# Kernel optimization log

Measured on AMD Instinct MI355X. Metric: run time of the kernel, lower is better.

Reference implementation:

```python
import jax, jax.numpy as jnp
import numpy as np


def _conv_same(x, k):
    # x: [C, H, W] single sample; k: [C_out, C_in, 3, 3] per-sample kernel
    return jax.lax.conv_general_dilated(
        x[None], k, window_strides=(1, 1), padding='SAME',
        dimension_numbers=('NCHW', 'OIHW', 'NCHW'))[0]


_batched_conv = jax.vmap(_conv_same)  # maps over batch of inputs and batch of kernels


def setup_inputs() -> dict:
    key = jax.random.key(0)
    k1, k2, k3 = jax.random.split(key, 3)
    B, C, H, W = 16, 256, 64, 64
    x = jax.random.normal(k1, (B, C, H, W), dtype=jnp.float32)
    # scale kernels down so pre-relu activations stay in a sane range
    kernel1 = jax.random.normal(k2, (B, C, C, 3, 3), dtype=jnp.float32) * 0.02
    kernel2 = jax.random.normal(k3, (B, C, C, 3, 3), dtype=jnp.float32) * 0.02
    return {"x": x, "kernel1": kernel1, "kernel2": kernel2}


def reference(x, kernel1, kernel2):
    # per-sample conv1 -> relu -> per-sample conv2 -> residual add -> relu
    h = jax.nn.relu(_batched_conv(x, kernel1))          # [B, C, H, W]
    out = jax.nn.relu(x + _batched_conv(h, kernel2))    # [B, C, H, W]
    return out
```

## Files before the change

### kernel.cpp

```cpp
#include <hip/hip_runtime.h>
#include <hip/hip_bf16.h>
#include <stdint.h>

typedef __attribute__((ext_vector_type(8))) short bf16x8;
typedef __attribute__((ext_vector_type(4))) float f32x4;
typedef __attribute__((address_space(1))) const void g_void;
typedef __attribute__((address_space(3))) void l_void;

#define NB 16
#define NC 256
#define NHW 4096
#define NT 72
#define ASLOT 8192
#define KSLOT 8192
#define SLOTB (ASLOT + KSLOT)

__global__ __launch_bounds__(256) void prep_xt2(const float* __restrict__ x,
                                                __hip_bfloat16* __restrict__ xt2) {
  __shared__ float tile[64][65];
  const int b = blockIdx.z;
  const int cb = blockIdx.y << 6;
  const int pb = blockIdx.x << 6;
  const float* xs = x + ((size_t)(b * NC + cb) << 12) + pb;
#pragma unroll
  for (int k = 0; k < 16; ++k) {
    int idx = threadIdx.x + (k << 8);
    int c = idx >> 6, p = idx & 63;
    tile[p][c] = xs[((size_t)c << 12) + p];
  }
  __syncthreads();
#pragma unroll
  for (int k = 0; k < 16; ++k) {
    int idx = threadIdx.x + (k << 8);
    int p = idx >> 6, c = idx & 63;
    int P = pb + p, C = cb + c;
    xt2[((size_t)(b * 8 + (C >> 5)) << 17) + ((size_t)P << 5) + (C & 31)] =
        __float2bfloat16(tile[p][c]);
  }
}

__global__ __launch_bounds__(256) void prep_kt2(const float* __restrict__ kin,
                                                __hip_bfloat16* __restrict__ kt2) {
  const int bco = blockIdx.x;
  const int b = bco >> 8, co = bco & 255;
  const size_t base = (size_t)bco * 2304;
  const int ci = threadIdx.x;
  float v[9];
#pragma unroll
  for (int s = 0; s < 9; ++s) v[s] = kin[base + ci * 9 + s];
  const int cib = ci >> 5, chunk = (ci >> 3) & 3, e = ci & 7;
  const int row = co & 127, ct = co >> 7;
  const int sc = chunk ^ ((row >> 1) & 3);
#pragma unroll
  for (int s = 0; s < 9; ++s) {
    const size_t dst = (((size_t)(b * 2 + ct) * NT + (cib * 9 + s)) << 12) +
                       (row << 5) + (sc << 3) + e;
    kt2[dst] = __float2bfloat16(v[s]);
  }
}

__global__ void zero_zp(float* zp) { zp[blockIdx.x * 256 + threadIdx.x] = 0.f; }

template <int PASS>
__global__ __launch_bounds__(256, 3) void conv_gemm(
    const __hip_bfloat16* __restrict__ img2,
    const __hip_bfloat16* __restrict__ kt2,
    const float* __restrict__ xres,
    const __hip_bfloat16* __restrict__ zp,
    void* __restrict__ outp) {
  __shared__ __align__(16) char L[3 * SLOTB];

  const int tid = threadIdx.x;
  const int lane = tid & 63;
  const int wid = tid >> 6;
  const int wm = wid >> 1, wn = wid & 1;

  const int orig = blockIdx.x;
  const int g = ((orig & 7) << 7) + (orig >> 3);
  const int b = g >> 6;
  const int t = g & 63;
  const int ptile = t >> 1;
  const int ct = t & 1;
  const int pbase = ptile << 7;

  const char* xb = (const char*)img2 + ((size_t)b << 21);
  const char* ktb = (const char*)kt2 + (((size_t)(b * 2 + ct) * NT) << 13);
  const char* zpb = (const char*)zp;

  const int srow = lane >> 2;
  const int sch = (lane & 3) ^ ((srow >> 1) & 3);

  const int wI = (PASS == 1) ? wm : wn;
  const int wK = (PASS == 1) ? wn : wm;
  int ioff[4], koff[4];
#pragma unroll
  for (int f = 0; f < 4; ++f) {
    const int ir = (wI << 6) + (f << 4) + (lane & 15);
    ioff[f] = (ir << 6) + ((((lane >> 4) ^ ((ir >> 1) & 3))) << 4);
    const int kr = (wK << 6) + (f << 4) + (lane & 15);
    koff[f] = (kr << 6) + ((((lane >> 4) ^ ((kr >> 1) & 3))) << 4);
  }
  const bool killlo = (lane & 15) == 0;
  const bool killhi = (lane & 15) == 15;
  const bf16x8 z8 = {0, 0, 0, 0, 0, 0, 0, 0};

  f32x4 acc[4][4];
#pragma unroll
  for (int i = 0; i < 4; ++i)
#pragma unroll
    for (int j = 0; j < 4; ++j) acc[i][j] = (f32x4){0.f, 0.f, 0.f, 0.f};

  auto stageA = [&](int slot, int cibp, int dh, int dw, bool dummy) {
    const char* cb = xb + ((size_t)(cibp & 7) << 18);
#pragma unroll
    for (int i = 0; i < 2; ++i) {
      const int grp = (i << 2) + wid;
      const int h = (ptile << 1) + (grp >> 2) + dh;
      const bool ok = !dummy && ((unsigned)h < 64u);
      const int off = ((pbase + (grp << 4) + srow + (dh << 6) + dw) << 6) + (sch << 4);
      const char* src = ok ? cb + off : zpb + (lane << 4);
      __builtin_amdgcn_global_load_lds((g_void*)src,
                                       (l_void*)(L + slot * SLOTB + (grp << 10)), 16, 0, 0);
    }
  };
  auto stageK = [&](int slot, int tn) {
    const char* src0 = ktb + ((size_t)tn << 13);
#pragma unroll
    for (int i = 0; i < 2; ++i) {
      const int grp = (i << 2) + wid;
      const char* src = (tn < NT) ? src0 + (grp << 10) + (lane << 4) : zpb + (lane << 4);
      __builtin_amdgcn_global_load_lds(
          (g_void*)src, (l_void*)(L + slot * SLOTB + ASLOT + (grp << 10)), 16, 0, 0);
    }
  };

  stageA(0, 0, -1, -1, false);
  stageK(0, 0);
  stageA(1, 0, -1, 0, false);
  stageK(1, 1);

#pragma unroll 1
  for (int cib = 0; cib < 8; ++cib) {
#pragma unroll
    for (int s = 0; s < 9; ++s) {
      const int kk = cib * 9 + s;
      asm volatile("s_waitcnt vmcnt(4)" ::: "memory");
      __builtin_amdgcn_s_barrier();
      {
        const int s2 = (s + 2) % 9;
        const int cib2 = cib + (s + 2) / 9;
        const int tn = kk + 2;
        stageA(tn % 3, cib2, s2 / 3 - 1, s2 % 3 - 1, tn >= NT);
        stageK(tn % 3, tn);
      }

      const char* As = L + (kk % 3) * SLOTB;
      const char* Ks = As + ASLOT;
      bf16x8 fi[4], fk[4];
#pragma unroll
      for (int f = 0; f < 4; ++f) fi[f] = *(const bf16x8*)(As + ioff[f]);
#pragma unroll
      for (int f = 0; f < 4; ++f) fk[f] = *(const bf16x8*)(Ks + koff[f]);
      const int dw = s % 3 - 1;
      if (dw == 1) fi[3] = killhi ? z8 : fi[3];
      if (dw == -1) fi[0] = killlo ? z8 : fi[0];

#pragma unroll
      for (int i = 0; i < 4; ++i)
#pragma unroll
        for (int j = 0; j < 4; ++j) {
          if (PASS == 1)
            acc[i][j] = __builtin_amdgcn_mfma_f32_16x16x32_bf16(fi[i], fk[j], acc[i][j], 0, 0, 0);
          else
            acc[i][j] = __builtin_amdgcn_mfma_f32_16x16x32_bf16(fk[i], fi[j], acc[i][j], 0, 0, 0);
        }
    }
  }
  asm volatile("s_waitcnt vmcnt(0)" ::: "memory");
  __builtin_amdgcn_sched_barrier(0);

  const int lg = lane >> 4;
  const int ln = lane & 15;
  if (PASS == 1) {
    __hip_bfloat16* ho = (__hip_bfloat16*)outp;
#pragma unroll
    for (int i = 0; i < 4; ++i)
#pragma unroll
      for (int j = 0; j < 4; ++j)
#pragma unroll
        for (int r = 0; r < 4; ++r) {
          int pixel = pbase + (wm << 6) + (i << 4) + (lg << 2) + r;
          int co = (ct << 7) + (wn << 6) + (j << 4) + ln;
          float v = acc[i][j][r];
          v = v > 0.f ? v : 0.f;
          ho[((size_t)(b * 8 + (co >> 5)) << 17) + ((size_t)pixel << 5) + (co & 31)] =
              __float2bfloat16(v);
        }
  } else {
    float* oo = (float*)outp;
#pragma unroll
    for (int i = 0; i < 4; ++i)
#pragma unroll
      for (int j = 0; j < 4; ++j)
#pragma unroll
        for (int r = 0; r < 4; ++r) {
          int co = (ct << 7) + (wm << 6) + (i << 4) + (lg << 2) + r;
          int pixel = pbase + (wn << 6) + (j << 4) + ln;
          size_t idx = ((size_t)(b * NC + co) << 12) + pixel;
          float v = acc[i][j][r] + xres[idx];
          oo[idx] = v > 0.f ? v : 0.f;
        }
  }
}

extern "C" void kernel_launch(void* const* d_in, const int* in_sizes, int n_in,
                              void* d_out, int out_size, void* d_ws, size_t ws_size,
                              hipStream_t stream) {
  const float* x = (const float*)d_in[0];
  const float* k1 = (const float*)d_in[1];
  const float* k2 = (const float*)d_in[2];

  char* w = (char*)d_ws;
  __hip_bfloat16* xt2 = (__hip_bfloat16*)(w + 256);
  __hip_bfloat16* ht2 = xt2 + (size_t)NB * 8 * NHW * 32;
  __hip_bfloat16* kt2 = ht2 + (size_t)NB * 8 * NHW * 32;
  float* zp = (float*)(kt2 + (size_t)NB * 2 * NT * 128 * 32);

  zero_zp<<<dim3(8), 256, 0, stream>>>(zp);
  prep_xt2<<<dim3(64, 4, NB), 256, 0, stream>>>(x, xt2);
  prep_kt2<<<dim3(NB * NC), 256, 0, stream>>>(k1, kt2);
  conv_gemm<1><<<dim3(1024), 256, 0, stream>>>(xt2, kt2, nullptr,
                                               (const __hip_bfloat16*)zp, (void*)ht2);
  prep_kt2<<<dim3(NB * NC), 256, 0, stream>>>(k2, kt2);
  conv_gemm<2><<<dim3(1024), 256, 0, stream>>>(ht2, kt2, x,
                                               (const __hip_bfloat16*)zp, d_out);
}
```

Before: 191.8 us.

## Load per-wave M operand directly to registers, share only N tile via LDS

Restructures the conv GEMM so each wave owns a 32-row slice of M and reads its M fragments straight from global memory into registers, double-buffered one step ahead. Only the N operand is staged through LDS, which halves shared memory per block and allows raising launch bounds to 4 blocks per SM. A wave now computes a 2x8 fragment grid instead of 4x4, and MFMA issue is wrapped in s_setprio. The cost is uncoalesced-ish direct global loads for the M side, which each wave must fetch without sharing, and more LDS reads of the B tile per wave.

New measurement: 241.7 us. +26.0%, slower.

```diff
diff --git a/kernel.cpp b/kernel.cpp
--- a/kernel.cpp
+++ b/kernel.cpp
@@ -11,9 +11,7 @@
 #define NC 256
 #define NHW 4096
 #define NT 72
-#define ASLOT 8192
-#define KSLOT 8192
-#define SLOTB (ASLOT + KSLOT)
+#define NSLOT 8192
 
 __global__ __launch_bounds__(256) void prep_xt2(const float* __restrict__ x,
                                                 __hip_bfloat16* __restrict__ xt2) {
@@ -62,18 +60,17 @@
 __global__ void zero_zp(float* zp) { zp[blockIdx.x * 256 + threadIdx.x] = 0.f; }
 
 template <int PASS>
-__global__ __launch_bounds__(256, 3) void conv_gemm(
+__global__ __launch_bounds__(256, 4) void conv_gemm(
     const __hip_bfloat16* __restrict__ img2,
     const __hip_bfloat16* __restrict__ kt2,
     const float* __restrict__ xres,
     const __hip_bfloat16* __restrict__ zp,
     void* __restrict__ outp) {
-  __shared__ __align__(16) char L[3 * SLOTB];
+  __shared__ __align__(16) char L[3 * NSLOT];
 
   const int tid = threadIdx.x;
   const int lane = tid & 63;
   const int wid = tid >> 6;
-  const int wm = wid >> 1, wn = wid & 1;
 
   const int orig = blockIdx.x;
   const int g = ((orig & 7) << 7) + (orig >> 3);
@@ -90,90 +87,124 @@
   const int srow = lane >> 2;
   const int sch = (lane & 3) ^ ((srow >> 1) & 3);
 
-  const int wI = (PASS == 1) ? wm : wn;
-  const int wK = (PASS == 1) ? wn : wm;
-  int ioff[4], koff[4];
-#pragma unroll
-  for (int f = 0; f < 4; ++f) {
-    const int ir = (wI << 6) + (f << 4) + (lane & 15);
-    ioff[f] = (ir << 6) + ((((lane >> 4) ^ ((ir >> 1) & 3))) << 4);
-    const int kr = (wK << 6) + (f << 4) + (lane & 15);
-    koff[f] = (kr << 6) + ((((lane >> 4) ^ ((kr >> 1) & 3))) << 4);
-  }
+  const int chk = (lane >> 4) << 4;
+  int pm[2], krowoff[2];
+#pragma unroll
+  for (int f = 0; f < 2; ++f) {
+    const int rM = (wid << 5) + (f << 4) + (lane & 15);
+    pm[f] = pbase + rM;
+    krowoff[f] = (rM << 6) + (((lane >> 4) ^ ((rM >> 1) & 3)) << 4);
+  }
+  int boff[8];
+#pragma unroll
+  for (int j = 0; j < 8; ++j) {
+    const int cj = (j << 4) + (lane & 15);
+    boff[j] = (cj << 6) + (((lane >> 4) ^ ((cj >> 1) & 3)) << 4);
+  }
+  const bool killAlo = ((wid & 1) == 0) && ((lane & 15) == 0);
+  const bool killAhi = ((wid & 1) == 1) && ((lane & 15) == 15);
   const bool killlo = (lane & 15) == 0;
   const bool killhi = (lane & 15) == 15;
   const bf16x8 z8 = {0, 0, 0, 0, 0, 0, 0, 0};
 
-  f32x4 acc[4][4];
-#pragma unroll
-  for (int i = 0; i < 4; ++i)
-#pragma unroll
-    for (int j = 0; j < 4; ++j) acc[i][j] = (f32x4){0.f, 0.f, 0.f, 0.f};
-
-  auto stageA = [&](int slot, int cibp, int dh, int dw, bool dummy) {
-    const char* cb = xb + ((size_t)(cibp & 7) << 18);
-#pragma unroll
-    for (int i = 0; i < 2; ++i) {
-      const int grp = (i << 2) + wid;
-      const int h = (ptile << 1) + (grp >> 2) + dh;
-      const bool ok = !dummy && ((unsigned)h < 64u);
-      const int off = ((pbase + (grp << 4) + srow + (dh << 6) + dw) << 6) + (sch << 4);
-      const char* src = ok ? cb + off : zpb + (lane << 4);
-      __builtin_amdgcn_global_load_lds((g_void*)src,
-                                       (l_void*)(L + slot * SLOTB + (grp << 10)), 16, 0, 0);
+  f32x4 acc[2][8];
+#pragma unroll
+  for (int i = 0; i < 2; ++i)
+#pragma unroll
+    for (int j = 0; j < 8; ++j) acc[i][j] = (f32x4){0.f, 0.f, 0.f, 0.f};
+
+  auto stageN = [&](int tn, int slot, int s2) {
+    char* dstb = L + slot * NSLOT;
+    if (PASS == 1) {
+      const char* src0 = ktb + ((size_t)tn << 13);
+#pragma unroll
+      for (int i = 0; i < 2; ++i) {
+        const int grp = (i << 2) + wid;
+        const char* src = (tn < NT) ? src0 + (grp << 10) + (lane << 4) : zpb + (lane << 4);
+        __builtin_amdgcn_global_load_lds((g_void*)src, (l_void*)(dstb + (grp << 10)), 16, 0, 0);
+      }
+    } else {
+      const int dh = s2 / 3 - 1, dw = s2 % 3 - 1;
+      const char* cb = xb + ((size_t)((tn / 9) & 7) << 18);
+      const bool dummy = tn >= NT;
+#pragma unroll
+      for (int i = 0; i < 2; ++i) {
+        const int grp = (i << 2) + wid;
+        const int h = (ptile << 1) + (grp >> 2) + dh;
+        const bool ok = !dummy && ((unsigned)h < 64u);
+        const int off = ((pbase + (grp << 4) + srow + (dh << 6) + dw) << 6) + (sch << 4);
+        const char* src = ok ? cb + off : zpb + (lane << 4);
+        __builtin_amdgcn_global_load_lds((g_void*)src, (l_void*)(dstb + (grp << 10)), 16, 0, 0);
+      }
     }
   };
-  auto stageK = [&](int slot, int tn) {
-    const char* src0 = ktb + ((size_t)tn << 13);
-#pragma unroll
-    for (int i = 0; i < 2; ++i) {
-      const int grp = (i << 2) + wid;
-      const char* src = (tn < NT) ? src0 + (grp << 10) + (lane << 4) : zpb + (lane << 4);
-      __builtin_amdgcn_global_load_lds(
-          (g_void*)src, (l_void*)(L + slot * SLOTB + ASLOT + (grp << 10)), 16, 0, 0);
+
+  auto loadM = [&](int tn, int s, bf16x8* dst) {
+    if (PASS == 1) {
+      const int tap = (s / 3 - 1) * 64 + (s % 3 - 1);
+      const char* cb = xb + ((size_t)((tn / 9) & 7) << 18);
+#pragma unroll
+      for (int f = 0; f < 2; ++f) {
+        const int pr = pm[f] + tap;
+        const bool ok = (tn < NT) && ((unsigned)pr < 4096u);
+        const char* src = ok ? cb + ((size_t)pr << 6) + chk : zpb + chk;
+        dst[f] = *(const bf16x8*)src;
+      }
+    } else {
+      const char* kb = ktb + ((size_t)tn << 13);
+#pragma unroll
+      for (int f = 0; f < 2; ++f) {
+        const char* src = (tn < NT) ? kb + krowoff[f] : zpb + chk;
+        dst[f] = *(const bf16x8*)src;
+      }
     }
   };
 
-  stageA(0, 0, -1, -1, false);
-  stageK(0, 0);
-  stageA(1, 0, -1, 0, false);
-  stageK(1, 1);
+  stageN(0, 0, 0);
+  stageN(1, 1, 1);
+  bf16x8 m0[2], m1[2];
+  loadM(0, 0, m0);
 
 #pragma unroll 1
-  for (int cib = 0; cib < 8; ++cib) {
-#pragma unroll
-    for (int s = 0; s < 9; ++s) {
-      const int kk = cib * 9 + s;
-      asm volatile("s_waitcnt vmcnt(4)" ::: "memory");
+  for (int t18 = 0; t18 < 4; ++t18) {
+    const int base = t18 * 18;
+#pragma unroll
+    for (int u = 0; u < 18; ++u) {
+      const int kk = base + u;
+      const int s = u % 9;
+      asm volatile("s_waitcnt vmcnt(2)" ::: "memory");
       __builtin_amdgcn_s_barrier();
-      {
-        const int s2 = (s + 2) % 9;
-        const int cib2 = cib + (s + 2) / 9;
-        const int tn = kk + 2;
-        stageA(tn % 3, cib2, s2 / 3 - 1, s2 % 3 - 1, tn >= NT);
-        stageK(tn % 3, tn);
-      }
-
-      const char* As = L + (kk % 3) * SLOTB;
-      const char* Ks = As + ASLOT;
-      bf16x8 fi[4], fk[4];
-#pragma unroll
-      for (int f = 0; f < 4; ++f) fi[f] = *(const bf16x8*)(As + ioff[f]);
-#pragma unroll
-      for (int f = 0; f < 4; ++f) fk[f] = *(const bf16x8*)(Ks + koff[f]);
+      stageN(kk + 2, (u + 2) % 3, (u + 2) % 9);
+      bf16x8* cur = (u & 1) ? m1 : m0;
+      bf16x8* nxt = (u & 1) ? m0 : m1;
+      loadM(kk + 1, (u + 1) % 9, nxt);
+
+      const char* Ns = L + (u % 3) * NSLOT;
       const int dw = s % 3 - 1;
-      if (dw == 1) fi[3] = killhi ? z8 : fi[3];
-      if (dw == -1) fi[0] = killlo ? z8 : fi[0];
-
-#pragma unroll
-      for (int i = 0; i < 4; ++i)
+      bf16x8 a0 = cur[0], a1 = cur[1];
+      if (PASS == 1) {
+        if (dw == -1) a0 = killAlo ? z8 : a0;
+        if (dw == 1) a1 = killAhi ? z8 : a1;
+      }
+#pragma unroll
+      for (int half = 0; half < 2; ++half) {
+        bf16x8 fb[4];
+#pragma unroll
+        for (int j = 0; j < 4; ++j) fb[j] = *(const bf16x8*)(Ns + boff[(half << 2) + j]);
+        if (PASS == 2) {
+          if (dw == -1) fb[0] = killlo ? z8 : fb[0];
+          if (dw == 1) fb[3] = killhi ? z8 : fb[3];
+        }
+        __builtin_amdgcn_s_setprio(1);
 #pragma unroll
         for (int j = 0; j < 4; ++j) {
-          if (PASS == 1)
-            acc[i][j] = __builtin_amdgcn_mfma_f32_16x16x32_bf16(fi[i], fk[j], acc[i][j], 0, 0, 0);
-          else
-            acc[i][j] = __builtin_amdgcn_mfma_f32_16x16x32_bf16(fk[i], fi[j], acc[i][j], 0, 0, 0);
-        }
+          acc[0][(half << 2) + j] =
+              __builtin_amdgcn_mfma_f32_16x16x32_bf16(a0, fb[j], acc[0][(half << 2) + j], 0, 0, 0);
+          acc[1][(half << 2) + j] =
+              __builtin_amdgcn_mfma_f32_16x16x32_bf16(a1, fb[j], acc[1][(half << 2) + j], 0, 0, 0);
+        }
+        __builtin_amdgcn_s_setprio(0);
+      }
     }
   }
   asm volatile("s_waitcnt vmcnt(0)" ::: "memory");
@@ -184,13 +215,13 @@
   if (PASS == 1) {
     __hip_bfloat16* ho = (__hip_bfloat16*)outp;
 #pragma unroll
-    for (int i = 0; i < 4; ++i)
-#pragma unroll
-      for (int j = 0; j < 4; ++j)
+    for (int i = 0; i < 2; ++i)
+#pragma unroll
+      for (int j = 0; j < 8; ++j)
 #pragma unroll
         for (int r = 0; r < 4; ++r) {
-          int pixel = pbase + (wm << 6) + (i << 4) + (lg << 2) + r;
-          int co = (ct << 7) + (wn << 6) + (j << 4) + ln;
+          int pixel = pbase + (wid << 5) + (i << 4) + (lg << 2) + r;
+          int co = (ct << 7) + (j << 4) + ln;
           float v = acc[i][j][r];
           v = v > 0.f ? v : 0.f;
           ho[((size_t)(b * 8 + (co >> 5)) << 17) + ((size_t)pixel << 5) + (co & 31)] =
@@ -199,13 +230,13 @@
   } else {
     float* oo = (float*)outp;
 #pragma unroll
-    for (int i = 0; i < 4; ++i)
-#pragma unroll
-      for (int j = 0; j < 4; ++j)
+    for (int i = 0; i < 2; ++i)
+#pragma unroll
+      for (int j = 0; j < 8; ++j)
 #pragma unroll
         for (int r = 0; r < 4; ++r) {
-          int co = (ct << 7) + (wm << 6) + (i << 4) + (lg << 2) + r;
-          int pixel = pbase + (wn << 6) + (j << 4) + ln;
+          int co = (ct << 7) + (wid << 5) + (i << 4) + (lg << 2) + r;
+          int pixel = pbase + (j << 4) + ln;
           size_t idx = ((size_t)(b * NC + co) << 12) + pixel;
           float v = acc[i][j][r] + xres[idx];
           oo[idx] = v > 0.f ? v : 0.f;
```

## Shrink LDS ring to double-buffer A, triple-buffer K; raise occupancy to 4

Applied to the files above, without the earlier changes.

Reshapes the conv GEMM pipeline so activation tiles are double-buffered with prefetch distance 1 while kernel tiles stay triple-buffered at distance 2. LDS per block drops from 48KB to 40KB, and launch bounds request 4 blocks per CU instead of 3. The main loop is unrolled over 18 steps so the slot indices fold to constants, and the wait threshold drops to vmcnt(2). It also folds the zero-page init into prep_xt2, removing one kernel launch. The shorter A prefetch distance may expose more load latency, and the higher occupancy target may force register spills.

New measurement: 262.8 us. 37.0% more time.

```diff
diff --git a/kernel.cpp b/kernel.cpp
--- a/kernel.cpp
+++ b/kernel.cpp
@@ -11,16 +11,19 @@
 #define NC 256
 #define NHW 4096
 #define NT 72
-#define ASLOT 8192
-#define KSLOT 8192
-#define SLOTB (ASLOT + KSLOT)
+#define TSLOT 8192
 
 __global__ __launch_bounds__(256) void prep_xt2(const float* __restrict__ x,
-                                                __hip_bfloat16* __restrict__ xt2) {
+                                                __hip_bfloat16* __restrict__ xt2,
+                                                float* __restrict__ zp) {
   __shared__ float tile[64][65];
   const int b = blockIdx.z;
   const int cb = blockIdx.y << 6;
   const int pb = blockIdx.x << 6;
+  if (blockIdx.x == 0 && blockIdx.y == 0 && blockIdx.z == 0) {
+#pragma unroll
+    for (int q = 0; q < 8; ++q) zp[(q << 8) + threadIdx.x] = 0.f;
+  }
   const float* xs = x + ((size_t)(b * NC + cb) << 12) + pb;
 #pragma unroll
   for (int k = 0; k < 16; ++k) {
@@ -59,16 +62,14 @@
   }
 }
 
-__global__ void zero_zp(float* zp) { zp[blockIdx.x * 256 + threadIdx.x] = 0.f; }
-
 template <int PASS>
-__global__ __launch_bounds__(256, 3) void conv_gemm(
+__global__ __launch_bounds__(256, 4) void conv_gemm(
     const __hip_bfloat16* __restrict__ img2,
     const __hip_bfloat16* __restrict__ kt2,
     const float* __restrict__ xres,
     const __hip_bfloat16* __restrict__ zp,
     void* __restrict__ outp) {
-  __shared__ __align__(16) char L[3 * SLOTB];
+  __shared__ __align__(16) char L[5 * TSLOT];
 
   const int tid = threadIdx.x;
   const int lane = tid & 63;
@@ -120,7 +121,7 @@
       const int off = ((pbase + (grp << 4) + srow + (dh << 6) + dw) << 6) + (sch << 4);
       const char* src = ok ? cb + off : zpb + (lane << 4);
       __builtin_amdgcn_global_load_lds((g_void*)src,
-                                       (l_void*)(L + slot * SLOTB + (grp << 10)), 16, 0, 0);
+                                       (l_void*)(L + slot * TSLOT + (grp << 10)), 16, 0, 0);
     }
   };
   auto stageK = [&](int slot, int tn) {
@@ -130,32 +131,32 @@
       const int grp = (i << 2) + wid;
       const char* src = (tn < NT) ? src0 + (grp << 10) + (lane << 4) : zpb + (lane << 4);
       __builtin_amdgcn_global_load_lds(
-          (g_void*)src, (l_void*)(L + slot * SLOTB + ASLOT + (grp << 10)), 16, 0, 0);
+          (g_void*)src, (l_void*)(L + (2 + slot) * TSLOT + (grp << 10)), 16, 0, 0);
     }
   };
 
+  stageK(0, 0);
   stageA(0, 0, -1, -1, false);
-  stageK(0, 0);
-  stageA(1, 0, -1, 0, false);
   stageK(1, 1);
 
 #pragma unroll 1
-  for (int cib = 0; cib < 8; ++cib) {
-#pragma unroll
-    for (int s = 0; s < 9; ++s) {
-      const int kk = cib * 9 + s;
-      asm volatile("s_waitcnt vmcnt(4)" ::: "memory");
+  for (int t18 = 0; t18 < 4; ++t18) {
+    const int base = t18 * 18;
+#pragma unroll
+    for (int u = 0; u < 18; ++u) {
+      const int kk = base + u;
+      const int s = u % 9;
+      asm volatile("s_waitcnt vmcnt(2)" ::: "memory");
       __builtin_amdgcn_s_barrier();
       {
-        const int s2 = (s + 2) % 9;
-        const int cib2 = cib + (s + 2) / 9;
-        const int tn = kk + 2;
-        stageA(tn % 3, cib2, s2 / 3 - 1, s2 % 3 - 1, tn >= NT);
-        stageK(tn % 3, tn);
+        const int s1 = (u + 1) % 9;
+        const int cib1 = (kk + 1) / 9;
+        stageA((u + 1) & 1, cib1, s1 / 3 - 1, s1 % 3 - 1, kk + 1 >= NT);
+        stageK((u + 2) % 3, kk + 2);
       }
 
-      const char* As = L + (kk % 3) * SLOTB;
-      const char* Ks = As + ASLOT;
+      const char* As = L + (u & 1) * TSLOT;
+      const char* Ks = L + (2 + u % 3) * TSLOT;
       bf16x8 fi[4], fk[4];
 #pragma unroll
       for (int f = 0; f < 4; ++f) fi[f] = *(const bf16x8*)(As + ioff[f]);
@@ -226,8 +227,7 @@
   __hip_bfloat16* kt2 = ht2 + (size_t)NB * 8 * NHW * 32;
   float* zp = (float*)(kt2 + (size_t)NB * 2 * NT * 128 * 32);
 
-  zero_zp<<<dim3(8), 256, 0, stream>>>(zp);
-  prep_xt2<<<dim3(64, 4, NB), 256, 0, stream>>>(x, xt2);
+  prep_xt2<<<dim3(64, 4, NB), 256, 0, stream>>>(x, xt2, zp);
   prep_kt2<<<dim3(NB * NC), 256, 0, stream>>>(k1, kt2);
   conv_gemm<1><<<dim3(1024), 256, 0, stream>>>(xt2, kt2, nullptr,
                                                (const __hip_bfloat16*)zp, (void*)ht2);
```
